# Kernel optimization log

Measured on AMD Instinct MI355X. Metric: run time of the kernel, lower is better.

Reference implementation:

```python
import jax, jax.numpy as jnp
import numpy as np

DELTA_V = 0.5
DELTA_D = 1.5
KSEG = 17  # segment ids 0..16 (0 = background)
EPS = 1e-12


def setup_inputs() -> dict:
    key = jax.random.key(0)
    k1, k2, k3 = jax.random.split(key, 3)
    B, C, H, W = 8, 8, 512, 512
    embeddings = jax.random.normal(k1, (B, C, H, W), dtype=jnp.float32)
    instance_labels = jax.random.randint(k2, (B, H, W), 0, KSEG, dtype=jnp.int32)
    mask = jax.random.randint(k3, (B, H, W), 0, 2, dtype=jnp.int32)
    return {"embeddings": embeddings, "instance_labels": instance_labels, "mask": mask}


def _discriminative_loss(embeddings, inst):
    # embeddings: (B, C, H, W); inst: (B, H, W) int, 0 = ignore/background
    B, C, H, W = embeddings.shape
    N = H * W
    ids = inst.reshape(B, N)
    # global segment ids so one segment_sum handles all batches
    gids = (ids + jnp.arange(B, dtype=ids.dtype)[:, None] * KSEG).reshape(-1)  # (B*N,)
    e = embeddings.reshape(B, C, N).transpose(0, 2, 1).reshape(B * N, C)       # (B*N, C)

    counts = jax.ops.segment_sum(jnp.ones((B * N,), embeddings.dtype), gids, num_segments=B * KSEG)
    sums = jax.ops.segment_sum(e, gids, num_segments=B * KSEG)                 # (B*KSEG, C)
    means = sums / jnp.maximum(counts, 1.0)[:, None]

    # ---- pull: per-pixel hinged distance to its instance mean ----
    diff = e - means[gids]                                                      # (B*N, C)
    d = jnp.sqrt(jnp.maximum(jnp.sum(diff * diff, axis=-1), EPS))               # (B*N,)
    pen = jnp.maximum(d - DELTA_V, 0.0) ** 2
    pen_mean = jax.ops.segment_sum(pen, gids, num_segments=B * KSEG) / jnp.maximum(counts, 1.0)

    counts_bk = counts.reshape(B, KSEG)
    pen_mean_bk = pen_mean.reshape(B, KSEG)
    present = (counts_bk > 0) & (jnp.arange(KSEG)[None, :] != 0)                # (B, KSEG) bool
    presentf = present.astype(embeddings.dtype)
    K = presentf.sum(axis=-1)                                                   # (B,) instances per image
    pull_b = (pen_mean_bk * presentf).sum(axis=-1) / jnp.maximum(K, 1.0)

    # ---- push: hinged pairwise mean distances ----
    mu = means.reshape(B, KSEG, C)
    dm = mu[:, :, None, :] - mu[:, None, :, :]                                  # (B, K, K, C)
    dist = jnp.sqrt(jnp.maximum(jnp.sum(dm * dm, axis=-1), EPS))
    hinge = jnp.maximum(2.0 * DELTA_D - dist, 0.0) ** 2
    iu = jnp.triu(jnp.ones((KSEG, KSEG), bool), k=1)                            # i < j
    pair_mask = (present[:, :, None] & present[:, None, :] & iu[None]).astype(embeddings.dtype)
    n_pairs = pair_mask.sum(axis=(-1, -2))
    push_b = (hinge * pair_mask).sum(axis=(-1, -2)) / jnp.maximum(n_pairs, 1.0)

    validf = (K > 0).astype(embeddings.dtype)
    nvalid = jnp.maximum(validf.sum(), 1.0)
    loss_pull = (pull_b * validf).sum() / nvalid
    loss_push = (push_b * validf).sum() / nvalid
    return loss_pull, loss_push


def reference(embeddings, instance_labels, mask):
    inst = instance_labels * mask  # zero out non-TCL pixels
    return _discriminative_loss(embeddings, inst)
```

## Files before the change

### kernel.cpp

```cpp
#include <hip/hip_runtime.h>

#define BATCH 8
#define CCH 8
#define HW 262144
#define SEGS 16


__global__ __launch_bounds__(256) void accum_kernel(
    const float* __restrict__ emb, const int* __restrict__ lab,
    const int* __restrict__ msk, float* __restrict__ ws)
{
    const int b = blockIdx.y;
    const int wave = threadIdx.x >> 6;
    __shared__ float lsum[4][SEGS][CCH];
    __shared__ float lcnt[4][SEGS];
    for (int i = threadIdx.x; i < 4 * SEGS * CCH; i += 256) (&lsum[0][0][0])[i] = 0.f;
    for (int i = threadIdx.x; i < 4 * SEGS; i += 256) (&lcnt[0][0])[i] = 0.f;
    __syncthreads();

    const float* eb = emb + (size_t)b * CCH * HW;
    const int4* lb = (const int4*)(lab + (size_t)b * HW);
    const int4* mb = (const int4*)(msk + (size_t)b * HW);

    const int ng = HW / 4;
    for (int g = blockIdx.x * 256 + threadIdx.x; g < ng; g += gridDim.x * 256) {
        int4 l4 = lb[g];
        int4 m4 = mb[g];
        int id[4];
        id[0] = m4.x ? l4.x : 0;
        id[1] = m4.y ? l4.y : 0;
        id[2] = m4.z ? l4.z : 0;
        id[3] = m4.w ? l4.w : 0;
#pragma unroll
        for (int j = 0; j < 4; ++j)
            if (id[j]) atomicAdd(&lcnt[wave][id[j] - 1], 1.0f);
#pragma unroll
        for (int c = 0; c < CCH; ++c) {
            float4 e4 = ((const float4*)(eb + (size_t)c * HW))[g];
            float ev[4] = {e4.x, e4.y, e4.z, e4.w};
#pragma unroll
            for (int j = 0; j < 4; ++j)
                if (id[j]) atomicAdd(&lsum[wave][id[j] - 1][c], ev[j]);
        }
    }
    __syncthreads();
    for (int i = threadIdx.x; i < SEGS * CCH; i += 256) {
        float v = (&lsum[0][0][0])[i] + (&lsum[1][0][0])[i]
                + (&lsum[2][0][0])[i] + (&lsum[3][0][0])[i];
        if (v != 0.f) atomicAdd(&ws[128 + b * SEGS * CCH + i], v);
    }
    for (int i = threadIdx.x; i < SEGS; i += 256) {
        float v = lcnt[0][i] + lcnt[1][i] + lcnt[2][i] + lcnt[3][i];
        if (v != 0.f) atomicAdd(&ws[b * SEGS + i], v);
    }
}

__global__ __launch_bounds__(256) void pull_kernel(
    const float* __restrict__ emb, const int* __restrict__ lab,
    const int* __restrict__ msk, float* __restrict__ ws)
{
    const int b = blockIdx.y;
    const int wave = threadIdx.x >> 6;
    __shared__ float mt[CCH][SEGS];
    __shared__ float lpen[4][SEGS];
    for (int i = threadIdx.x; i < 4 * SEGS; i += 256) (&lpen[0][0])[i] = 0.f;
    if (threadIdx.x < SEGS * CCH) {
        int s = threadIdx.x & (SEGS - 1);
        int c = threadIdx.x >> 4;
        float cnt = ws[b * SEGS + s];
        mt[c][s] = ws[128 + (b * SEGS + s) * CCH + c] / fmaxf(cnt, 1.0f);
    }
    __syncthreads();

    const float* eb = emb + (size_t)b * CCH * HW;
    const int4* lb = (const int4*)(lab + (size_t)b * HW);
    const int4* mb = (const int4*)(msk + (size_t)b * HW);

    const int ng = HW / 4;
    for (int g = blockIdx.x * 256 + threadIdx.x; g < ng; g += gridDim.x * 256) {
        int4 l4 = lb[g];
        int4 m4 = mb[g];
        int id[4];
        id[0] = m4.x ? l4.x : 0;
        id[1] = m4.y ? l4.y : 0;
        id[2] = m4.z ? l4.z : 0;
        id[3] = m4.w ? l4.w : 0;
        int ix[4];
#pragma unroll
        for (int j = 0; j < 4; ++j) ix[j] = id[j] ? id[j] - 1 : 0;
        float ss[4] = {0.f, 0.f, 0.f, 0.f};
#pragma unroll
        for (int c = 0; c < CCH; ++c) {
            float4 e4 = ((const float4*)(eb + (size_t)c * HW))[g];
            float ev[4] = {e4.x, e4.y, e4.z, e4.w};
#pragma unroll
            for (int j = 0; j < 4; ++j) {
                float d = ev[j] - mt[c][ix[j]];
                ss[j] += d * d;
            }
        }
#pragma unroll
        for (int j = 0; j < 4; ++j) {
            if (id[j]) {
                float d = sqrtf(fmaxf(ss[j], 1e-12f));
                float h = fmaxf(d - 0.5f, 0.f);
                atomicAdd(&lpen[wave][ix[j]], h * h);
            }
        }
    }
    __syncthreads();
    for (int i = threadIdx.x; i < SEGS; i += 256) {
        float v = lpen[0][i] + lpen[1][i] + lpen[2][i] + lpen[3][i];
        if (v != 0.f) atomicAdd(&ws[1152 + b * SEGS + i], v);
    }
}

__global__ __launch_bounds__(256) void finalize_kernel(
    const float* __restrict__ ws, float* __restrict__ out)
{
    __shared__ float cnt[BATCH][SEGS];
    __shared__ float mu[BATCH][SEGS][CCH];
    __shared__ float pen[BATCH][SEGS];
    __shared__ float res[BATCH][3];

    for (int i = threadIdx.x; i < BATCH * SEGS; i += 256) {
        (&cnt[0][0])[i] = ws[i];
        (&pen[0][0])[i] = ws[1152 + i];
    }
    for (int i = threadIdx.x; i < BATCH * SEGS * CCH; i += 256) {
        float c = ws[i / CCH];
        (&mu[0][0][0])[i] = ws[128 + i] / fmaxf(c, 1.0f);
    }
    __syncthreads();

    const int b = threadIdx.x >> 5;
    const int l = threadIdx.x & 31;

    float pullv = 0.f, Kf = 0.f;
    if (l < SEGS && cnt[b][l] > 0.f) {
        Kf = 1.f;
        pullv = pen[b][l] / cnt[b][l];
    }
    float hs = 0.f, np = 0.f;
    for (int p = l; p < 256; p += 32) {
        int i = p >> 4, j = p & 15;
        if (i < j && cnt[b][i] > 0.f && cnt[b][j] > 0.f) {
            float ssq = 0.f;
#pragma unroll
            for (int c = 0; c < CCH; ++c) {
                float d = mu[b][i][c] - mu[b][j][c];
                ssq += d * d;
            }
            float dist = sqrtf(fmaxf(ssq, 1e-12f));
            float h = fmaxf(3.0f - dist, 0.f);
            hs += h * h;
            np += 1.f;
        }
    }
#pragma unroll
    for (int m = 16; m >= 1; m >>= 1) {
        pullv += __shfl_xor(pullv, m);
        Kf    += __shfl_xor(Kf, m);
        hs    += __shfl_xor(hs, m);
        np    += __shfl_xor(np, m);
    }
    if (l == 0) {
        res[b][0] = (Kf > 0.f) ? pullv / Kf : 0.f;
        res[b][1] = (np > 0.f) ? hs / np : 0.f;
        res[b][2] = (Kf > 0.f) ? 1.f : 0.f;
    }
    __syncthreads();
    if (threadIdx.x == 0) {
        float sp = 0.f, sh = 0.f, nv = 0.f;
        for (int bb = 0; bb < BATCH; ++bb) {
            sp += res[bb][0] * res[bb][2];
            sh += res[bb][1] * res[bb][2];
            nv += res[bb][2];
        }
        nv = fmaxf(nv, 1.f);
        out[0] = sp / nv;
        out[1] = sh / nv;
    }
}

extern "C" void kernel_launch(void* const* d_in, const int* in_sizes, int n_in,
                              void* d_out, int out_size, void* d_ws, size_t ws_size,
                              hipStream_t stream)
{
    const float* emb = (const float*)d_in[0];
    const int* lab = (const int*)d_in[1];
    const int* msk = (const int*)d_in[2];
    float* out = (float*)d_out;
    float* ws = (float*)d_ws;

    hipMemsetAsync(d_ws, 0, 1280 * sizeof(float), stream);
    dim3 grid(128, BATCH);
    accum_kernel<<<grid, 256, 0, stream>>>(emb, lab, msk, ws);
    pull_kernel<<<grid, 256, 0, stream>>>(emb, lab, msk, ws);
    finalize_kernel<<<1, 256, 0, stream>>>(ws, out);
}
```

Baseline: 157.3 us.

## Replace shared-memory atomics with register one-hot accumulation and wave reductions

Both the accumulation and pull kernels drop per-wave LDS atomicAdd histograms. Each thread now keeps per-segment partial sums in registers, updated through one-hot FMA selects, and reduces them across the wave with shuffles before issuing global atomics. In accum, each wave handles two channels, so every wave re-reads the labels and mask while splitting the embedding reads by channel. This removes contended LDS atomics but adds 16x select/FMA work per pixel and raises register pressure.

```diff
diff --git a/kernel.cpp b/kernel.cpp
--- a/kernel.cpp
+++ b/kernel.cpp
@@ -4,6 +4,7 @@
 #define CCH 8
 #define HW 262144
 #define SEGS 16
+#define GX 128
 
 
 __global__ __launch_bounds__(256) void accum_kernel(
@@ -12,46 +13,65 @@
 {
     const int b = blockIdx.y;
     const int wave = threadIdx.x >> 6;
-    __shared__ float lsum[4][SEGS][CCH];
-    __shared__ float lcnt[4][SEGS];
-    for (int i = threadIdx.x; i < 4 * SEGS * CCH; i += 256) (&lsum[0][0][0])[i] = 0.f;
-    for (int i = threadIdx.x; i < 4 * SEGS; i += 256) (&lcnt[0][0])[i] = 0.f;
-    __syncthreads();
+    const int lane = threadIdx.x & 63;
+    const int c0 = wave * 2;
+
+    float s0[SEGS], s1[SEGS], cnt[SEGS];
+#pragma unroll
+    for (int s = 0; s < SEGS; ++s) { s0[s] = 0.f; s1[s] = 0.f; cnt[s] = 0.f; }
 
     const float* eb = emb + (size_t)b * CCH * HW;
     const int4* lb = (const int4*)(lab + (size_t)b * HW);
     const int4* mb = (const int4*)(msk + (size_t)b * HW);
+    const float4* ep0 = (const float4*)(eb + (size_t)c0 * HW);
+    const float4* ep1 = (const float4*)(eb + (size_t)(c0 + 1) * HW);
 
     const int ng = HW / 4;
-    for (int g = blockIdx.x * 256 + threadIdx.x; g < ng; g += gridDim.x * 256) {
-        int4 l4 = lb[g];
-        int4 m4 = mb[g];
-        int id[4];
-        id[0] = m4.x ? l4.x : 0;
-        id[1] = m4.y ? l4.y : 0;
-        id[2] = m4.z ? l4.z : 0;
-        id[3] = m4.w ? l4.w : 0;
-#pragma unroll
-        for (int j = 0; j < 4; ++j)
-            if (id[j]) atomicAdd(&lcnt[wave][id[j] - 1], 1.0f);
-#pragma unroll
-        for (int c = 0; c < CCH; ++c) {
-            float4 e4 = ((const float4*)(eb + (size_t)c * HW))[g];
-            float ev[4] = {e4.x, e4.y, e4.z, e4.w};
-#pragma unroll
-            for (int j = 0; j < 4; ++j)
-                if (id[j]) atomicAdd(&lsum[wave][id[j] - 1][c], ev[j]);
-        }
-    }
-    __syncthreads();
-    for (int i = threadIdx.x; i < SEGS * CCH; i += 256) {
-        float v = (&lsum[0][0][0])[i] + (&lsum[1][0][0])[i]
-                + (&lsum[2][0][0])[i] + (&lsum[3][0][0])[i];
-        if (v != 0.f) atomicAdd(&ws[128 + b * SEGS * CCH + i], v);
-    }
-    for (int i = threadIdx.x; i < SEGS; i += 256) {
-        float v = lcnt[0][i] + lcnt[1][i] + lcnt[2][i] + lcnt[3][i];
-        if (v != 0.f) atomicAdd(&ws[b * SEGS + i], v);
+    for (int base = blockIdx.x * 256; base < ng; base += GX * 256) {
+#pragma unroll
+        for (int q = 0; q < 4; ++q) {
+            const int g = base + (q << 6) + lane;
+            int4 l4 = lb[g];
+            int4 m4 = mb[g];
+            float4 ea = ep0[g];
+            float4 ec = ep1[g];
+            int id[4] = { m4.x ? l4.x : 0, m4.y ? l4.y : 0,
+                          m4.z ? l4.z : 0, m4.w ? l4.w : 0 };
+            float e0[4] = { ea.x, ea.y, ea.z, ea.w };
+            float e1[4] = { ec.x, ec.y, ec.z, ec.w };
+#pragma unroll
+            for (int j = 0; j < 4; ++j) {
+#pragma unroll
+                for (int s = 0; s < SEGS; ++s) {
+                    float oh = (id[j] == s + 1) ? 1.0f : 0.0f;
+                    cnt[s] += oh;
+                    s0[s] = fmaf(oh, e0[j], s0[s]);
+                    s1[s] = fmaf(oh, e1[j], s1[s]);
+                }
+            }
+        }
+    }
+
+#pragma unroll
+    for (int s = 0; s < SEGS; ++s) {
+#pragma unroll
+        for (int m = 32; m >= 1; m >>= 1) {
+            s0[s]  += __shfl_xor(s0[s], m);
+            s1[s]  += __shfl_xor(s1[s], m);
+            cnt[s] += __shfl_xor(cnt[s], m);
+        }
+    }
+    if (lane == 0) {
+#pragma unroll
+        for (int s = 0; s < SEGS; ++s) {
+            if (s0[s] != 0.f) atomicAdd(&ws[128 + (b * SEGS + s) * CCH + c0],     s0[s]);
+            if (s1[s] != 0.f) atomicAdd(&ws[128 + (b * SEGS + s) * CCH + c0 + 1], s1[s]);
+        }
+        if (wave == 0) {
+#pragma unroll
+            for (int s = 0; s < SEGS; ++s)
+                if (cnt[s] != 0.f) atomicAdd(&ws[b * SEGS + s], cnt[s]);
+        }
     }
 }
 
@@ -60,58 +80,65 @@
     const int* __restrict__ msk, float* __restrict__ ws)
 {
     const int b = blockIdx.y;
-    const int wave = threadIdx.x >> 6;
+    const int lane = threadIdx.x & 63;
     __shared__ float mt[CCH][SEGS];
-    __shared__ float lpen[4][SEGS];
-    for (int i = threadIdx.x; i < 4 * SEGS; i += 256) (&lpen[0][0])[i] = 0.f;
+
     if (threadIdx.x < SEGS * CCH) {
         int s = threadIdx.x & (SEGS - 1);
         int c = threadIdx.x >> 4;
-        float cnt = ws[b * SEGS + s];
-        mt[c][s] = ws[128 + (b * SEGS + s) * CCH + c] / fmaxf(cnt, 1.0f);
+        float cv = ws[b * SEGS + s];
+        mt[c][s] = ws[128 + (b * SEGS + s) * CCH + c] / fmaxf(cv, 1.0f);
     }
     __syncthreads();
+
+    float pens[SEGS];
+#pragma unroll
+    for (int s = 0; s < SEGS; ++s) pens[s] = 0.f;
 
     const float* eb = emb + (size_t)b * CCH * HW;
     const int4* lb = (const int4*)(lab + (size_t)b * HW);
     const int4* mb = (const int4*)(msk + (size_t)b * HW);
 
     const int ng = HW / 4;
-    for (int g = blockIdx.x * 256 + threadIdx.x; g < ng; g += gridDim.x * 256) {
+    for (int g = blockIdx.x * 256 + threadIdx.x; g < ng; g += GX * 256) {
         int4 l4 = lb[g];
         int4 m4 = mb[g];
-        int id[4];
-        id[0] = m4.x ? l4.x : 0;
-        id[1] = m4.y ? l4.y : 0;
-        id[2] = m4.z ? l4.z : 0;
-        id[3] = m4.w ? l4.w : 0;
+        int id[4] = { m4.x ? l4.x : 0, m4.y ? l4.y : 0,
+                      m4.z ? l4.z : 0, m4.w ? l4.w : 0 };
         int ix[4];
 #pragma unroll
         for (int j = 0; j < 4; ++j) ix[j] = id[j] ? id[j] - 1 : 0;
-        float ss[4] = {0.f, 0.f, 0.f, 0.f};
+        float ss[4] = { 0.f, 0.f, 0.f, 0.f };
 #pragma unroll
         for (int c = 0; c < CCH; ++c) {
             float4 e4 = ((const float4*)(eb + (size_t)c * HW))[g];
-            float ev[4] = {e4.x, e4.y, e4.z, e4.w};
+            float ev[4] = { e4.x, e4.y, e4.z, e4.w };
 #pragma unroll
             for (int j = 0; j < 4; ++j) {
                 float d = ev[j] - mt[c][ix[j]];
-                ss[j] += d * d;
+                ss[j] = fmaf(d, d, ss[j]);
             }
         }
 #pragma unroll
         for (int j = 0; j < 4; ++j) {
-            if (id[j]) {
-                float d = sqrtf(fmaxf(ss[j], 1e-12f));
-                float h = fmaxf(d - 0.5f, 0.f);
-                atomicAdd(&lpen[wave][ix[j]], h * h);
-            }
-        }
-    }
-    __syncthreads();
-    for (int i = threadIdx.x; i < SEGS; i += 256) {
-        float v = lpen[0][i] + lpen[1][i] + lpen[2][i] + lpen[3][i];
-        if (v != 0.f) atomicAdd(&ws[1152 + b * SEGS + i], v);
+            float d = sqrtf(fmaxf(ss[j], 1e-12f));
+            float h = fmaxf(d - 0.5f, 0.f);
+            float h2 = h * h;
+#pragma unroll
+            for (int s = 0; s < SEGS; ++s)
+                pens[s] += (id[j] == s + 1) ? h2 : 0.f;
+        }
+    }
+
+#pragma unroll
+    for (int s = 0; s < SEGS; ++s) {
+#pragma unroll
+        for (int m = 32; m >= 1; m >>= 1) pens[s] += __shfl_xor(pens[s], m);
+    }
+    if (lane == 0) {
+#pragma unroll
+        for (int s = 0; s < SEGS; ++s)
+            if (pens[s] != 0.f) atomicAdd(&ws[1152 + b * SEGS + s], pens[s]);
     }
 }
 
@@ -194,7 +221,7 @@
     float* ws = (float*)d_ws;
 
     hipMemsetAsync(d_ws, 0, 1280 * sizeof(float), stream);
-    dim3 grid(128, BATCH);
+    dim3 grid(GX, BATCH);
     accum_kernel<<<grid, 256, 0, stream>>>(emb, lab, msk, ws);
     pull_kernel<<<grid, 256, 0, stream>>>(emb, lab, msk, ws);
     finalize_kernel<<<1, 256, 0, stream>>>(ws, out);
```

Measured after the change: 460.3 us. 193% more time.
